# Optimization experiments

Hardware: AMD Instinct MI355X
Metric: run time of the kernel (lower is better)

The kernel has to match this reference:

```python
import jax, jax.numpy as jnp
import numpy as np

K, N = 8, 20          # exactly-K-of-N circuit
B = 524288            # batch
NEG = -1e9            # masked-softmax logit


def setup_inputs() -> dict:
    key = jax.random.key(0)
    k1, k2, k3 = jax.random.split(key, 3)
    # boolean data vector per example
    x = jax.random.randint(k1, (B, N), 0, 2).astype(bool)
    # leaf sum-node weights: node S(1, m) has m weights, stored in row m (padded to N)
    Wleaf = jax.random.uniform(k2, (N + 1, N), dtype=jnp.float32)
    # internal sum-node weights: node S(k, m) (1 < k < m <= N, incl. root) has 2 weights
    W2 = jax.random.uniform(k3, (K + 1, N + 1, 2), dtype=jnp.float32)
    return {"x": x, "Wleaf": Wleaf, "W2": W2}


def _circuit(xf, Wleaf, W2):
    """Tensorized DP over the (k, m) lattice; same math as the recursive circuit:
      S(m, m) = prod_{i<m} x_i                                (prodNode base case)
      S(1, m) = sum_i w_i * x_i * prod_{j<m, j!=i} (1 - x_j)  (leaf sumNode)
      S(k, m) = w0 * S(k, m-1) + w1 * S(k-1, m-1) * x_{m-1}   (internal sumNode)
    Root output = S(K, N), shape [B, 1].
    """
    Bsz = xf.shape[0]
    csum = jnp.cumsum(xf, axis=1)    # running count of ones
    pre = jnp.cumprod(xf, axis=1)    # pre[:, m-1] = prod_{i<m} x_i = S(m, m)

    # --- leaf row k = 1, vectorized over m ---
    mask = jnp.arange(N)[None, :] < jnp.arange(N + 1)[:, None]      # [N+1, N]
    wsm = jax.nn.softmax(jnp.where(mask, Wleaf, NEG), axis=-1)
    wsm = jnp.where(mask, wsm, 0.0)
    dots = xf @ wsm.T                                               # [B, N+1]: sum_{i<m} w_i x_i
    # for boolean x: x_i * prod_{j<m, j!=i}(1-x_j) is nonzero iff exactly one of
    # x[:, :m] is set, so S(1, m) = 1[count_m == 1] * (w . x[:, :m])
    exactly_one = jnp.concatenate(
        [jnp.zeros((Bsz, 1), xf.dtype), (csum == 1.0).astype(xf.dtype)], axis=1)
    S_cols = [exactly_one[:, m] * dots[:, m] for m in range(N + 1)]  # row k = 1

    # --- internal rows k = 2 .. K ---
    w2 = jax.nn.softmax(W2, axis=-1)   # softmax over each node's 2 children
    zero = jnp.zeros((Bsz,), xf.dtype)
    for k in range(2, K + 1):
        row = [zero] * (N + 1)
        row[k] = pre[:, k - 1]                      # S(k, k) = prod of first k inputs
        for m in range(k + 1, N + 1):
            row[m] = w2[k, m, 0] * row[m - 1] + w2[k, m, 1] * S_cols[m - 1] * xf[:, m - 1]
        S_cols = row
    return S_cols[N][:, None]    # [B, 1], like torch matmul output


def reference(x, Wleaf, W2):
    return _circuit(x.astype(jnp.float32), Wleaf, W2)
```

## Files before the change

kernel.cpp:

```cpp
#include <hip/hip_runtime.h>
#include <hip/hip_bf16.h>

static constexpr int NB  = 20;
static constexpr int KK  = 8;

__global__ __launch_bounds__(256) void pc_kernel(
    const void* __restrict__ xraw,
    const void* __restrict__ wleaf_raw,
    const void* __restrict__ w2_raw,
    void* __restrict__ outraw,
    int batch)
{
    __shared__ float s_wsm[(NB + 1) * NB];
    __shared__ float s_w20[(KK + 1) * (NB + 1)];
    __shared__ float s_w21[(KK + 1) * (NB + 1)];
    __shared__ int s_flagX;
    __shared__ int s_flagW;
    __shared__ int s_cntW;
    __shared__ int s_xKind;

    const int tid = threadIdx.x;

    if (tid == 0) { s_cntW = 0; s_xKind = 0; }
    __syncthreads();

    if (tid < 64) {
        unsigned v = ((const unsigned*)xraw)[tid];
        if (v > 1u) {
            if (((v & 0xFFFFu) == 0x3F80u) || ((v >> 16) == 0x3F80u))
                atomicOr(&s_xKind, 2);
            else
                atomicOr(&s_xKind, 1);
        }
    } else if (tid < 64 + 192) {
        unsigned v = ((const unsigned*)wleaf_raw)[tid - 64];
        unsigned hb = (v >> 8) & 0xFFu;
        if (hb >= 0x30u && hb <= 0x40u) atomicAdd(&s_cntW, 1);
    }
    __syncthreads();
    if (tid == 0) {
        int xk = s_xKind;
        s_flagX = (xk & 2) ? 2 : ((xk & 1) ? 1 : 0);
        s_flagW = (s_cntW > 96) ? 1 : 0;
    }
    __syncthreads();
    const int fX = s_flagX;
    const int fW = s_flagW;

    auto WL = [&](int idx) -> float {
        return fW ? __bfloat162float(((const __hip_bfloat16*)wleaf_raw)[idx])
                  : ((const float*)wleaf_raw)[idx];
    };
    auto W2v = [&](int idx) -> float {
        return fW ? __bfloat162float(((const __hip_bfloat16*)w2_raw)[idx])
                  : ((const float*)w2_raw)[idx];
    };

    if (tid >= 1 && tid <= NB) {
        const int m = tid;
        float mx = -1e30f;
        for (int i = 0; i < m; ++i) mx = fmaxf(mx, WL(m * NB + i));
        float s = 0.f;
        for (int i = 0; i < m; ++i) s += expf(WL(m * NB + i) - mx);
        const float inv = 1.f / s;
        for (int i = 0; i < m; ++i) s_wsm[m * NB + i] = expf(WL(m * NB + i) - mx) * inv;
    }
    if (tid >= 21 && tid < 21 + (KK + 1) * (NB + 1)) {
        const int idx = tid - 21;
        const float a = W2v(idx * 2 + 0);
        const float b = W2v(idx * 2 + 1);
        const float mx = fmaxf(a, b);
        const float ea = expf(a - mx), eb = expf(b - mx);
        const float inv = 1.f / (ea + eb);
        s_w20[idx] = ea * inv;
        s_w21[idx] = eb * inv;
    }
    __syncthreads();

    const int b = blockIdx.x * 256 + tid;
    if (b >= batch) return;

    unsigned bits = 0;
    if (fX == 0) {
        const int4* row = (const int4*)((const int*)xraw + (size_t)b * NB);
        #pragma unroll
        for (int j = 0; j < 5; ++j) {
            int4 v = row[j];
            bits |= (unsigned)(v.x != 0) << (4 * j + 0);
            bits |= (unsigned)(v.y != 0) << (4 * j + 1);
            bits |= (unsigned)(v.z != 0) << (4 * j + 2);
            bits |= (unsigned)(v.w != 0) << (4 * j + 3);
        }
    } else if (fX == 1) {
        const unsigned* p = (const unsigned*)((const unsigned char*)xraw + (size_t)b * NB);
        #pragma unroll
        for (int j = 0; j < 5; ++j) {
            unsigned v = p[j];
            bits |= (unsigned)(((v      ) & 0xFFu) != 0) << (4 * j + 0);
            bits |= (unsigned)(((v >>  8) & 0xFFu) != 0) << (4 * j + 1);
            bits |= (unsigned)(((v >> 16) & 0xFFu) != 0) << (4 * j + 2);
            bits |= (unsigned)(((v >> 24)       ) != 0) << (4 * j + 3);
        }
    } else {
        const unsigned* p = (const unsigned*)((const unsigned short*)xraw + (size_t)b * NB);
        #pragma unroll
        for (int j = 0; j < 10; ++j) {
            unsigned v = p[j];
            bits |= (unsigned)((v & 0xFFFFu) != 0) << (2 * j + 0);
            bits |= (unsigned)((v >> 16)     != 0) << (2 * j + 1);
        }
    }

    float S[NB + 1];
    S[0] = 0.f;
    int pc = 0;
    int onlyIdx = 0;
    #pragma unroll
    for (int m = 1; m <= NB; ++m) {
        if ((bits >> (m - 1)) & 1u) { pc++; onlyIdx = m - 1; }
        const float wv = s_wsm[m * NB + onlyIdx];
        S[m] = (pc == 1) ? wv : 0.f;
    }

    #pragma unroll
    for (int k = 2; k <= KK; ++k) {
        const unsigned lm = (1u << k) - 1u;
        float prevNew = ((bits & lm) == lm) ? 1.f : 0.f;
        float oldPrev = S[k];
        S[k] = prevNew;
        #pragma unroll
        for (int m = k + 1; m <= NB; ++m) {
            const float oldCur = S[m];
            const float t = ((bits >> (m - 1)) & 1u) ? oldPrev : 0.f;
            const float cur = fmaf(s_w20[k * (NB + 1) + m], prevNew,
                                   s_w21[k * (NB + 1) + m] * t);
            S[m] = cur;
            prevNew = cur;
            oldPrev = oldCur;
        }
    }

    if (fW) ((__hip_bfloat16*)outraw)[b] = __float2bfloat16(S[NB]);
    else    ((float*)outraw)[b]          = S[NB];
}

extern "C" void kernel_launch(void* const* d_in, const int* in_sizes, int n_in,
                              void* d_out, int out_size, void* d_ws, size_t ws_size,
                              hipStream_t stream) {
    (void)n_in; (void)d_ws; (void)ws_size;
    const int batch = in_sizes[0] / NB;
    const int blocks = (batch + 255) / 256;
    pc_kernel<<<blocks, 256, 0, stream>>>(d_in[0], d_in[1], d_in[2], d_out, batch);
}
```

Before: 91.64 us.

## Split circuit into low/high bit tables and combine with a 16-term dot product

```diff
diff --git a/kernel.cpp b/kernel.cpp
--- a/kernel.cpp
+++ b/kernel.cpp
@@ -3,48 +3,33 @@
 
 static constexpr int NB  = 20;
 static constexpr int KK  = 8;
-
-__global__ __launch_bounds__(256) void pc_kernel(
-    const void* __restrict__ xraw,
+static constexpr int MS  = 12;
+static constexpr int NLO = 1 << MS;
+static constexpr int NHI = 1 << (NB - MS);
+
+
+__global__ __launch_bounds__(256) void pc_tables(
     const void* __restrict__ wleaf_raw,
     const void* __restrict__ w2_raw,
-    void* __restrict__ outraw,
-    int batch)
+    float* __restrict__ tbl)
 {
     __shared__ float s_wsm[(NB + 1) * NB];
     __shared__ float s_w20[(KK + 1) * (NB + 1)];
     __shared__ float s_w21[(KK + 1) * (NB + 1)];
-    __shared__ int s_flagX;
-    __shared__ int s_flagW;
-    __shared__ int s_cntW;
-    __shared__ int s_xKind;
+    __shared__ int s_cntW, s_flagW;
 
     const int tid = threadIdx.x;
-
-    if (tid == 0) { s_cntW = 0; s_xKind = 0; }
-    __syncthreads();
-
-    if (tid < 64) {
-        unsigned v = ((const unsigned*)xraw)[tid];
-        if (v > 1u) {
-            if (((v & 0xFFFFu) == 0x3F80u) || ((v >> 16) == 0x3F80u))
-                atomicOr(&s_xKind, 2);
-            else
-                atomicOr(&s_xKind, 1);
-        }
-    } else if (tid < 64 + 192) {
-        unsigned v = ((const unsigned*)wleaf_raw)[tid - 64];
+    if (tid == 0) s_cntW = 0;
+    __syncthreads();
+
+    if (tid < 192) {
+        unsigned v = ((const unsigned*)wleaf_raw)[tid];
         unsigned hb = (v >> 8) & 0xFFu;
         if (hb >= 0x30u && hb <= 0x40u) atomicAdd(&s_cntW, 1);
     }
     __syncthreads();
-    if (tid == 0) {
-        int xk = s_xKind;
-        s_flagX = (xk & 2) ? 2 : ((xk & 1) ? 1 : 0);
-        s_flagW = (s_cntW > 96) ? 1 : 0;
-    }
-    __syncthreads();
-    const int fX = s_flagX;
+    if (tid == 0) s_flagW = (s_cntW > 96) ? 1 : 0;
+    __syncthreads();
     const int fW = s_flagW;
 
     auto WL = [&](int idx) -> float {
@@ -77,6 +62,122 @@
     }
     __syncthreads();
 
+    const int g = blockIdx.x * 256 + tid;
+    float e[16];
+
+    if (g < NLO) {
+        const unsigned bits = (unsigned)g;
+        float S[MS + 1];
+        S[0] = 0.f;
+        int pc = 0, onlyIdx = 0;
+        #pragma unroll
+        for (int m = 1; m <= MS; ++m) {
+            if ((bits >> (m - 1)) & 1u) { pc++; onlyIdx = m - 1; }
+            const float wv = s_wsm[m * NB + onlyIdx];
+            S[m] = (pc == 1) ? wv : 0.f;
+        }
+        e[0] = S[MS];
+        #pragma unroll
+        for (int k = 2; k <= KK; ++k) {
+            const unsigned lm = (1u << k) - 1u;
+            float prevNew = ((bits & lm) == lm) ? 1.f : 0.f;
+            float oldPrev = S[k];
+            S[k] = prevNew;
+            #pragma unroll
+            for (int m = k + 1; m <= MS; ++m) {
+                const float oldCur = S[m];
+                const float t = ((bits >> (m - 1)) & 1u) ? oldPrev : 0.f;
+                const float cur = fmaf(s_w20[k * (NB + 1) + m], prevNew,
+                                       s_w21[k * (NB + 1) + m] * t);
+                S[m] = cur; prevNew = cur; oldPrev = oldCur;
+            }
+            e[k - 1] = S[MS];
+        }
+        e[8] = (pc == 0) ? 1.f : 0.f;
+        #pragma unroll
+        for (int m = MS + 1; m <= NB - 1; ++m)
+            e[9 + m - (MS + 1)] = (pc == 1) ? s_wsm[m * NB + onlyIdx] : 0.f;
+    } else {
+        const unsigned H = (unsigned)(g - NLO);
+        float lam[KK + 2];
+        #pragma unroll
+        for (int k = 0; k <= KK + 1; ++k) lam[k] = 0.f;
+        lam[KK] = 1.f;
+        float wS1[NB];
+        #pragma unroll
+        for (int m = NB; m >= MS + 1; --m) {
+            const float fb = ((H >> (m - 1 - MS)) & 1u) ? 1.f : 0.f;
+            wS1[m - 1] = s_w21[2 * (NB + 1) + m] * fb * lam[2];
+            float nl[KK + 1];
+            #pragma unroll
+            for (int k = 2; k <= KK - 1; ++k)
+                nl[k] = fmaf(s_w20[k * (NB + 1) + m], lam[k],
+                             s_w21[(k + 1) * (NB + 1) + m] * (fb * lam[k + 1]));
+            nl[KK] = s_w20[KK * (NB + 1) + m] * lam[KK];
+            #pragma unroll
+            for (int k = 2; k <= KK; ++k) lam[k] = nl[k];
+        }
+        e[0] = wS1[MS];
+        #pragma unroll
+        for (int k = 2; k <= KK; ++k) e[k - 1] = lam[k];
+        float beta = 0.f;
+        #pragma unroll
+        for (int m = MS + 1; m <= NB - 1; ++m) {
+            const unsigned mask = (1u << (m - MS)) - 1u;
+            const unsigned sub = H & mask;
+            float phi = 0.f;
+            if (sub && !(sub & (sub - 1))) {
+                const int j = __builtin_ctz(sub);
+                phi = s_wsm[m * NB + MS + j];
+            }
+            beta = fmaf(phi, wS1[m], beta);
+            e[9 + m - (MS + 1)] = (sub == 0u) ? wS1[m] : 0.f;
+        }
+        e[8] = beta;
+    }
+
+    float4* dst = (float4*)(tbl + (size_t)g * 16);
+    dst[0] = make_float4(e[0],  e[1],  e[2],  e[3]);
+    dst[1] = make_float4(e[4],  e[5],  e[6],  e[7]);
+    dst[2] = make_float4(e[8],  e[9],  e[10], e[11]);
+    dst[3] = make_float4(e[12], e[13], e[14], e[15]);
+}
+
+__global__ __launch_bounds__(256) void pc_main(
+    const void* __restrict__ xraw,
+    const void* __restrict__ wleaf_raw,
+    void* __restrict__ outraw,
+    const float* __restrict__ tbl,
+    int batch)
+{
+    __shared__ int s_flagX, s_flagW, s_cntW, s_xKind;
+    const int tid = threadIdx.x;
+    if (tid == 0) { s_cntW = 0; s_xKind = 0; }
+    __syncthreads();
+
+    if (tid < 64) {
+        unsigned v = ((const unsigned*)xraw)[tid];
+        if (v > 1u) {
+            if (((v & 0xFFFFu) == 0x3F80u) || ((v >> 16) == 0x3F80u))
+                atomicOr(&s_xKind, 2);
+            else
+                atomicOr(&s_xKind, 1);
+        }
+    } else if (tid < 64 + 192) {
+        unsigned v = ((const unsigned*)wleaf_raw)[tid - 64];
+        unsigned hb = (v >> 8) & 0xFFu;
+        if (hb >= 0x30u && hb <= 0x40u) atomicAdd(&s_cntW, 1);
+    }
+    __syncthreads();
+    if (tid == 0) {
+        int xk = s_xKind;
+        s_flagX = (xk & 2) ? 2 : ((xk & 1) ? 1 : 0);
+        s_flagW = (s_cntW > 96) ? 1 : 0;
+    }
+    __syncthreads();
+    const int fX = s_flagX;
+    const int fW = s_flagW;
+
     const int b = blockIdx.x * 256 + tid;
     if (b >= batch) return;
 
@@ -111,44 +212,31 @@
         }
     }
 
-    float S[NB + 1];
-    S[0] = 0.f;
-    int pc = 0;
-    int onlyIdx = 0;
+    const float4* lp = (const float4*)tbl + (size_t)(bits & (unsigned)(NLO - 1)) * 4;
+    const float4* hp = (const float4*)(tbl + (size_t)NLO * 16) + (size_t)(bits >> MS) * 4;
+
+    float acc = 0.f;
     #pragma unroll
-    for (int m = 1; m <= NB; ++m) {
-        if ((bits >> (m - 1)) & 1u) { pc++; onlyIdx = m - 1; }
-        const float wv = s_wsm[m * NB + onlyIdx];
-        S[m] = (pc == 1) ? wv : 0.f;
-    }
-
-    #pragma unroll
-    for (int k = 2; k <= KK; ++k) {
-        const unsigned lm = (1u << k) - 1u;
-        float prevNew = ((bits & lm) == lm) ? 1.f : 0.f;
-        float oldPrev = S[k];
-        S[k] = prevNew;
-        #pragma unroll
-        for (int m = k + 1; m <= NB; ++m) {
-            const float oldCur = S[m];
-            const float t = ((bits >> (m - 1)) & 1u) ? oldPrev : 0.f;
-            const float cur = fmaf(s_w20[k * (NB + 1) + m], prevNew,
-                                   s_w21[k * (NB + 1) + m] * t);
-            S[m] = cur;
-            prevNew = cur;
-            oldPrev = oldCur;
-        }
-    }
-
-    if (fW) ((__hip_bfloat16*)outraw)[b] = __float2bfloat16(S[NB]);
-    else    ((float*)outraw)[b]          = S[NB];
+    for (int j = 0; j < 4; ++j) {
+        const float4 a = lp[j];
+        const float4 c = hp[j];
+        acc = fmaf(a.x, c.x, acc);
+        acc = fmaf(a.y, c.y, acc);
+        acc = fmaf(a.z, c.z, acc);
+        acc = fmaf(a.w, c.w, acc);
+    }
+
+    if (fW) ((__hip_bfloat16*)outraw)[b] = __float2bfloat16(acc);
+    else    ((float*)outraw)[b]          = acc;
 }
 
 extern "C" void kernel_launch(void* const* d_in, const int* in_sizes, int n_in,
                               void* d_out, int out_size, void* d_ws, size_t ws_size,
                               hipStream_t stream) {
-    (void)n_in; (void)d_ws; (void)ws_size;
+    (void)n_in; (void)out_size; (void)ws_size;
     const int batch = in_sizes[0] / NB;
+    float* tbl = (float*)d_ws;
+    pc_tables<<<(NLO + NHI) / 256, 256, 0, stream>>>(d_in[1], d_in[2], tbl);
     const int blocks = (batch + 255) / 256;
-    pc_kernel<<<blocks, 256, 0, stream>>>(d_in[0], d_in[1], d_in[2], d_out, batch);
+    pc_main<<<blocks, 256, 0, stream>>>(d_in[0], d_in[1], d_out, tbl, batch);
 }
```

Result: slower. 96.34 us (+5.1%).

## Process two rows per thread and issue input loads before weight softmax

Applied to the files above, without the earlier changes.

```diff
diff --git a/kernel.cpp b/kernel.cpp
--- a/kernel.cpp
+++ b/kernel.cpp
@@ -3,6 +3,7 @@
 
 static constexpr int NB  = 20;
 static constexpr int KK  = 8;
+static constexpr int EPT = 2;
 
 __global__ __launch_bounds__(256) void pc_kernel(
     const void* __restrict__ xraw,
@@ -14,10 +15,8 @@
     __shared__ float s_wsm[(NB + 1) * NB];
     __shared__ float s_w20[(KK + 1) * (NB + 1)];
     __shared__ float s_w21[(KK + 1) * (NB + 1)];
-    __shared__ int s_flagX;
-    __shared__ int s_flagW;
-    __shared__ int s_cntW;
-    __shared__ int s_xKind;
+    __shared__ float s_inv[NB + 1];
+    __shared__ int s_flagX, s_flagW, s_cntW, s_xKind;
 
     const int tid = threadIdx.x;
 
@@ -56,16 +55,62 @@
                   : ((const float*)w2_raw)[idx];
     };
 
+    const int base = blockIdx.x * (256 * EPT) + tid;
+    unsigned bits[EPT];
+    bool valid[EPT];
+    #pragma unroll
+    for (int e = 0; e < EPT; ++e) {
+        const int b = base + e * 256;
+        valid[e] = (b < batch);
+        unsigned bb = 0;
+        if (valid[e]) {
+            if (fX == 0) {
+                const int4* row = (const int4*)((const int*)xraw + (size_t)b * NB);
+                #pragma unroll
+                for (int j = 0; j < 5; ++j) {
+                    int4 v = row[j];
+                    bb |= (unsigned)(v.x != 0) << (4 * j + 0);
+                    bb |= (unsigned)(v.y != 0) << (4 * j + 1);
+                    bb |= (unsigned)(v.z != 0) << (4 * j + 2);
+                    bb |= (unsigned)(v.w != 0) << (4 * j + 3);
+                }
+            } else if (fX == 1) {
+                const unsigned* p = (const unsigned*)((const unsigned char*)xraw + (size_t)b * NB);
+                #pragma unroll
+                for (int j = 0; j < 5; ++j) {
+                    unsigned v = p[j];
+                    bb |= (unsigned)(((v      ) & 0xFFu) != 0) << (4 * j + 0);
+                    bb |= (unsigned)(((v >>  8) & 0xFFu) != 0) << (4 * j + 1);
+                    bb |= (unsigned)(((v >> 16) & 0xFFu) != 0) << (4 * j + 2);
+                    bb |= (unsigned)(((v >> 24)       ) != 0) << (4 * j + 3);
+                }
+            } else {
+                const unsigned* p = (const unsigned*)((const unsigned short*)xraw + (size_t)b * NB);
+                #pragma unroll
+                for (int j = 0; j < 10; ++j) {
+                    unsigned v = p[j];
+                    bb |= (unsigned)((v & 0xFFFFu) != 0) << (2 * j + 0);
+                    bb |= (unsigned)((v >> 16)     != 0) << (2 * j + 1);
+                }
+            }
+        }
+        bits[e] = bb;
+    }
+
+    if (tid < 200) {
+        #pragma unroll
+        for (int s = 0; s < 2; ++s) {
+            const int p = 20 + tid + s * 200;
+            const int m = p / 20, i = p - m * 20;
+            if (i < m) s_wsm[p] = expf(WL(p));
+        }
+    }
+    __syncthreads();
     if (tid >= 1 && tid <= NB) {
-        const int m = tid;
-        float mx = -1e30f;
-        for (int i = 0; i < m; ++i) mx = fmaxf(mx, WL(m * NB + i));
         float s = 0.f;
-        for (int i = 0; i < m; ++i) s += expf(WL(m * NB + i) - mx);
-        const float inv = 1.f / s;
-        for (int i = 0; i < m; ++i) s_wsm[m * NB + i] = expf(WL(m * NB + i) - mx) * inv;
-    }
-    if (tid >= 21 && tid < 21 + (KK + 1) * (NB + 1)) {
+        for (int i = 0; i < tid; ++i) s += s_wsm[tid * NB + i];
+        s_inv[tid] = 1.f / s;
+    } else if (tid >= 21 && tid < 21 + (KK + 1) * (NB + 1)) {
         const int idx = tid - 21;
         const float a = W2v(idx * 2 + 0);
         const float b = W2v(idx * 2 + 1);
@@ -76,79 +121,71 @@
         s_w21[idx] = eb * inv;
     }
     __syncthreads();
-
-    const int b = blockIdx.x * 256 + tid;
-    if (b >= batch) return;
-
-    unsigned bits = 0;
-    if (fX == 0) {
-        const int4* row = (const int4*)((const int*)xraw + (size_t)b * NB);
+    if (tid < 200) {
         #pragma unroll
-        for (int j = 0; j < 5; ++j) {
-            int4 v = row[j];
-            bits |= (unsigned)(v.x != 0) << (4 * j + 0);
-            bits |= (unsigned)(v.y != 0) << (4 * j + 1);
-            bits |= (unsigned)(v.z != 0) << (4 * j + 2);
-            bits |= (unsigned)(v.w != 0) << (4 * j + 3);
-        }
-    } else if (fX == 1) {
-        const unsigned* p = (const unsigned*)((const unsigned char*)xraw + (size_t)b * NB);
-        #pragma unroll
-        for (int j = 0; j < 5; ++j) {
-            unsigned v = p[j];
-            bits |= (unsigned)(((v      ) & 0xFFu) != 0) << (4 * j + 0);
-            bits |= (unsigned)(((v >>  8) & 0xFFu) != 0) << (4 * j + 1);
-            bits |= (unsigned)(((v >> 16) & 0xFFu) != 0) << (4 * j + 2);
-            bits |= (unsigned)(((v >> 24)       ) != 0) << (4 * j + 3);
-        }
-    } else {
-        const unsigned* p = (const unsigned*)((const unsigned short*)xraw + (size_t)b * NB);
-        #pragma unroll
-        for (int j = 0; j < 10; ++j) {
-            unsigned v = p[j];
-            bits |= (unsigned)((v & 0xFFFFu) != 0) << (2 * j + 0);
-            bits |= (unsigned)((v >> 16)     != 0) << (2 * j + 1);
+        for (int s = 0; s < 2; ++s) {
+            const int p = 20 + tid + s * 200;
+            const int m = p / 20, i = p - m * 20;
+            if (i < m) s_wsm[p] *= s_inv[m];
         }
     }
+    __syncthreads();
 
-    float S[NB + 1];
-    S[0] = 0.f;
-    int pc = 0;
-    int onlyIdx = 0;
+    float S[EPT][NB + 1];
+    int pc[EPT], oi[EPT];
+    #pragma unroll
+    for (int e = 0; e < EPT; ++e) { S[e][0] = 0.f; pc[e] = 0; oi[e] = 0; }
     #pragma unroll
     for (int m = 1; m <= NB; ++m) {
-        if ((bits >> (m - 1)) & 1u) { pc++; onlyIdx = m - 1; }
-        const float wv = s_wsm[m * NB + onlyIdx];
-        S[m] = (pc == 1) ? wv : 0.f;
+        #pragma unroll
+        for (int e = 0; e < EPT; ++e) {
+            if ((bits[e] >> (m - 1)) & 1u) { pc[e]++; oi[e] = m - 1; }
+            const float wv = s_wsm[m * NB + oi[e]];
+            S[e][m] = (pc[e] == 1) ? wv : 0.f;
+        }
     }
 
     #pragma unroll
     for (int k = 2; k <= KK; ++k) {
         const unsigned lm = (1u << k) - 1u;
-        float prevNew = ((bits & lm) == lm) ? 1.f : 0.f;
-        float oldPrev = S[k];
-        S[k] = prevNew;
+        float prevNew[EPT], oldPrev[EPT];
+        #pragma unroll
+        for (int e = 0; e < EPT; ++e) {
+            prevNew[e] = ((bits[e] & lm) == lm) ? 1.f : 0.f;
+            oldPrev[e] = S[e][k];
+            S[e][k] = prevNew[e];
+        }
         #pragma unroll
         for (int m = k + 1; m <= NB; ++m) {
-            const float oldCur = S[m];
-            const float t = ((bits >> (m - 1)) & 1u) ? oldPrev : 0.f;
-            const float cur = fmaf(s_w20[k * (NB + 1) + m], prevNew,
-                                   s_w21[k * (NB + 1) + m] * t);
-            S[m] = cur;
-            prevNew = cur;
-            oldPrev = oldCur;
+            const float w0 = s_w20[k * (NB + 1) + m];
+            const float w1 = s_w21[k * (NB + 1) + m];
+            #pragma unroll
+            for (int e = 0; e < EPT; ++e) {
+                const float oldCur = S[e][m];
+                const float t = ((bits[e] >> (m - 1)) & 1u) ? oldPrev[e] : 0.f;
+                const float cur = fmaf(w0, prevNew[e], w1 * t);
+                S[e][m] = cur;
+                prevNew[e] = cur;
+                oldPrev[e] = oldCur;
+            }
         }
     }
 
-    if (fW) ((__hip_bfloat16*)outraw)[b] = __float2bfloat16(S[NB]);
-    else    ((float*)outraw)[b]          = S[NB];
+    #pragma unroll
+    for (int e = 0; e < EPT; ++e) {
+        const int b = base + e * 256;
+        if (valid[e]) {
+            if (fW) ((__hip_bfloat16*)outraw)[b] = __float2bfloat16(S[e][NB]);
+            else    ((float*)outraw)[b]          = S[e][NB];
+        }
+    }
 }
 
 extern "C" void kernel_launch(void* const* d_in, const int* in_sizes, int n_in,
                               void* d_out, int out_size, void* d_ws, size_t ws_size,
                               hipStream_t stream) {
-    (void)n_in; (void)d_ws; (void)ws_size;
+    (void)n_in; (void)out_size; (void)d_ws; (void)ws_size;
     const int batch = in_sizes[0] / NB;
-    const int blocks = (batch + 255) / 256;
+    const int blocks = (batch + 256 * EPT - 1) / (256 * EPT);
     pc_kernel<<<blocks, 256, 0, stream>>>(d_in[0], d_in[1], d_in[2], d_out, batch);
 }
```

Result: no change. 89.85 us (-2.0%).
